# Optimization experiments

Measured on AMD Instinct MI355X. Metric: run time of the kernel, lower is better.

Reference implementation:

```python
import jax, jax.numpy as jnp
import numpy as np

# norse LIFParameters defaults with v_th overridden to 0.33
DT = 1e-3
TAU_SYN_INV = 200.0   # 1/5e-3
TAU_MEM_INV = 100.0   # 1/1e-2
V_TH = 0.33
ALPHA = 100.0         # SuperSpike surrogate slope
SEQ_LEN = 32

@jax.custom_vjp
def superspike(x):
    # Heaviside forward, SuperSpike surrogate backward (norse method='super')
    return (x > 0).astype(x.dtype)

def _ss_fwd(x):
    return superspike(x), x

def _ss_bwd(x, g):
    return (g / (ALPHA * jnp.abs(x) + 1.0) ** 2,)

superspike.defvjp(_ss_fwd, _ss_bwd)

def _encode(current):
    # ConstantCurrentLIFEncoder: LIF current encoder, constant input current
    def step(v, _):
        v = v + DT * TAU_MEM_INV * (-v + current)
        z = superspike(v - V_TH)
        v = v - z * v  # v_reset = 0
        return v, z
    _, spikes = jax.lax.scan(step, jnp.zeros_like(current), None, length=SEQ_LEN)
    return spikes  # [T, B, F]

def _lif_step(inp, v, i):
    # norse lif_feed_forward_step (v_leak=0, v_reset=0)
    v_dec = v + DT * TAU_MEM_INV * (-v + i)
    i_dec = i * (1.0 - DT * TAU_SYN_INV)
    z = superspike(v_dec - V_TH)
    return z, v_dec * (1.0 - z), i_dec + inp

def setup_inputs() -> dict:
    key = jax.random.key(0)
    ks = jax.random.split(key, 6)
    B, F_IN, N_CLASSES = 2048, 2048, 100  # F_IN = 2*input_size
    def lin_w(k, out_f, in_f):
        bound = 1.0 / np.sqrt(in_f)
        return jax.random.uniform(k, (out_f, in_f), jnp.float32, -bound, bound)
    return {
        "x": jax.random.normal(ks[0], (B, F_IN), jnp.float32),
        "w1": lin_w(ks[1], 512, F_IN),
        "w2": lin_w(ks[2], 512, 512),
        "w3": lin_w(ks[3], 256, 512),
        "w_out": lin_w(ks[4], N_CLASSES, 256),
        "feature_scalar": jnp.ones((1,), jnp.float32),
        "encoder_scalar": jnp.ones((1,), jnp.float32),
    }

def reference(x, w1, w2, w3, w_out, feature_scalar, encoder_scalar):
    B = x.shape[0]
    n_classes = w_out.shape[0]
    # encoder + scaling (dropout is identity in eval mode)
    spikes = 5.0 * encoder_scalar * _encode(2.0 * feature_scalar * x)  # [T,B,F]

    def step(carry, z_t):
        v1, i1, v2, i2, v3, i3, vo, io = carry
        s1, v1, i1 = _lif_step(z_t @ w1.T, v1, i1)
        s2, v2, i2 = _lif_step(s1 @ w2.T, v2, i2)
        s3, v3, i3 = _lif_step(s2 @ w3.T, v3, i3)
        # LILinearCell (leaky integrator, no spike)
        vo = vo + DT * TAU_MEM_INV * (-vo + io)
        io = io * (1.0 - DT * TAU_SYN_INV) + s3 @ w_out.T
        return (v1, i1, v2, i2, v3, i3, vo, io), None

    z = lambda *s: jnp.zeros(s, x.dtype)
    init = (z(B, 512), z(B, 512), z(B, 512), z(B, 512),
            z(B, 256), z(B, 256), z(B, n_classes), z(B, n_classes))
    final, _ = jax.lax.scan(step, init, spikes)
    # decode = voltages[-1] == LI membrane voltage at last timestep
    return final[6]
```

## Files before the change

kernel.cpp:

```cpp
#include <hip/hip_runtime.h>
#include <cstddef>


#define THREADS 256

typedef float f4v __attribute__((ext_vector_type(4)));
typedef float f2v __attribute__((ext_vector_type(2)));

__device__ __forceinline__ void gl_lds16(const float* g, float* l) {
#if __has_builtin(__builtin_amdgcn_global_load_lds)
  __builtin_amdgcn_global_load_lds(
      (const __attribute__((address_space(1))) void*)g,
      (__attribute__((address_space(3))) void*)l, 16, 0, 0);
#else
  *(float4*)l = *(const float4*)g;
#endif
}

#define WOFF1 0
#define WOFF2 1048576
#define WOFF3 1310720
#define WOFF4 1441792
#define WTOT  1474560

__global__ __launch_bounds__(THREADS) void prep_kernel(
    const float* __restrict__ w1, const float* __restrict__ w2,
    const float* __restrict__ w3, const float* __restrict__ w4,
    float* __restrict__ wt)
{
  int idx = blockIdx.x * THREADS + threadIdx.x;
  if (idx >= WTOT) return;
  if (idx < WOFF2) {
    int j = idx >> 9, o = idx & 511;
    wt[idx] = w1[o * 2048 + j];
  } else if (idx < WOFF3) {
    int r = idx - WOFF2, j = r >> 9, o = r & 511;
    wt[idx] = w2[o * 512 + j];
  } else if (idx < WOFF4) {
    int r = idx - WOFF3, j = r >> 8, o = r & 255;
    wt[idx] = w3[o * 512 + j];
  } else {
    int r = idx - WOFF4, j = r >> 7, o = r & 127;
    wt[idx] = (o < 100) ? w4[o * 256 + j] : 0.0f;
  }
}

__global__ __launch_bounds__(THREADS) void enc_kernel(
    const float* __restrict__ x, const float* __restrict__ fscale,
    unsigned* __restrict__ em, int b0)
{
  int idx = blockIdx.x * THREADS + threadIdx.x;
  int b = idx >> 11, j = idx & 2047;
  float c = 2.0f * fscale[0] * x[((size_t)(b0 + b) << 11) + j];
  float v = 0.0f;
  unsigned m = 0u;
#pragma unroll
  for (int t = 0; t < 32; ++t) {
    v = v + 0.1f * (c - v);
    unsigned z = ((v - 0.33f) > 0.0f) ? 1u : 0u;
    m |= z << t;
    if (z) v = 0.0f;
  }
  em[idx] = m;
}

template <int O, bool FINAL>
__global__ __launch_bounds__(THREADS, 2) void gemm_sparse(
    const unsigned* __restrict__ mIn, const float* __restrict__ WT,
    int J, const float* __restrict__ es,
    unsigned* __restrict__ mOut, float* __restrict__ out, int bbase)
{
  constexpr int NAO = (O >= 256) ? 4 : 2;
  constexpr int WPB = O / (64 * NAO);
  constexpr int BPB = 4 / WPB;
  constexpr int BK  = 8192 / O;
  constexpr int CH  = 8192;
  static_assert(BK % 4 == 0, "uint4 mask loads");
  __shared__ float lds[2 * CH];
  const int tid = threadIdx.x;
  const int lane = tid & 63, wvid = tid >> 6;
  const int b = blockIdx.x * BPB + wvid / WPB;
  const int obase = (wvid % WPB) * (64 * NAO) + lane * NAO;
  const int nb = J / BK;
  float scalef = es ? 5.0f * es[0] : 1.0f;
  const int scale_i =
      __builtin_amdgcn_readfirstlane(__float_as_int(scalef));
  float* const buf0 = lds;
  float* const buf1 = lds + CH;

  float acc[32][NAO];
#pragma unroll
  for (int t = 0; t < 32; ++t)
#pragma unroll
    for (int k = 0; k < NAO; ++k) acc[t][k] = 0.0f;

  const unsigned* mrow = mIn + (size_t)b * J;

  auto stage = [&](int cb, float* buf) {
#pragma unroll
    for (int i = 0; i < CH / THREADS / 4; ++i) {
      int flat = (tid + i * THREADS) * 4;
      gl_lds16(WT + (size_t)cb * CH + flat, buf + flat);
    }
  };

  auto fma_chunk = [&](int cb, const float* buf) {
    uint4 mw[BK / 4];
#pragma unroll
    for (int q = 0; q < BK / 4; ++q)
      mw[q] = ((const uint4*)(mrow + cb * BK))[q];
    unsigned mwa[BK];
#pragma unroll
    for (int q = 0; q < BK / 4; ++q) {
      mwa[4 * q + 0] = mw[q].x; mwa[4 * q + 1] = mw[q].y;
      mwa[4 * q + 2] = mw[q].z; mwa[4 * q + 3] = mw[q].w;
    }
#pragma unroll
    for (int j = 0; j < BK; ++j) {
      const unsigned w =
          (unsigned)__builtin_amdgcn_readfirstlane((int)mwa[j]);
      if (w) {
        if constexpr (NAO == 4) {
          const f4v wv = *(const f4v*)(buf + j * O + obase);
#pragma unroll
          for (int t = 0; t < 32; ++t) {
            float av = __int_as_float(
                (int)((((int)(w << (31 - t))) >> 31) & scale_i));
#pragma unroll
            for (int k = 0; k < 4; ++k)
              acc[t][k] = fmaf(av, wv[k], acc[t][k]);
          }
        } else {
          const f2v wv = *(const f2v*)(buf + j * O + obase);
#pragma unroll
          for (int t = 0; t < 32; ++t) {
            float av = __int_as_float(
                (int)((((int)(w << (31 - t))) >> 31) & scale_i));
#pragma unroll
            for (int k = 0; k < 2; ++k)
              acc[t][k] = fmaf(av, wv[k], acc[t][k]);
          }
        }
      }
    }
  };

  stage(0, buf0);
  for (int cb = 0; cb < nb; cb += 2) {
    __syncthreads();
    if (cb + 1 < nb) stage(cb + 1, buf1);
    fma_chunk(cb, buf0);
    __syncthreads();
    if (cb + 2 < nb) stage(cb + 2, buf0);
    fma_chunk(cb + 1, buf1);
  }

#pragma unroll
  for (int k = 0; k < NAO; ++k) {
    if (FINAL) {
      float v = 0.0f, cur = 0.0f;
#pragma unroll
      for (int t2 = 0; t2 < 32; ++t2) {
        v = v + 0.1f * (cur - v);
        cur = 0.8f * cur + acc[t2][k];
      }
      int o = obase + k;
      if (o < 100) out[(size_t)(bbase + b) * 100 + o] = v;
    } else {
      float v = 0.0f, cur = 0.0f;
      unsigned zw = 0u;
#pragma unroll
      for (int t2 = 0; t2 < 32; ++t2) {
        v = v + 0.1f * (cur - v);
        unsigned z = ((v - 0.33f) > 0.0f) ? 1u : 0u;
        zw |= z << t2;
        if (z) v = 0.0f;
        cur = 0.8f * cur + acc[t2][k];
      }
      mOut[(size_t)b * O + obase + k] = zw;
    }
  }
}

extern "C" void kernel_launch(void* const* d_in, const int* in_sizes, int n_in,
                              void* d_out, int out_size, void* d_ws, size_t ws_size,
                              hipStream_t stream)
{
  const float* x  = (const float*)d_in[0];
  const float* w1 = (const float*)d_in[1];
  const float* w2 = (const float*)d_in[2];
  const float* w3 = (const float*)d_in[3];
  const float* w4 = (const float*)d_in[4];
  const float* fs = (const float*)d_in[5];
  const float* es = (const float*)d_in[6];
  float* out = (float*)d_out;
  (void)in_sizes; (void)n_in; (void)out_size;

  int Bc = 2048;
  auto need = [](int bc) -> size_t {
    return ((size_t)WTOT + (size_t)bc * (2048 + 512 + 512 + 256)) * 4;
  };
  while (Bc > 64 && need(Bc) > ws_size) Bc >>= 1;

  float* WT = (float*)d_ws;
  unsigned* em  = (unsigned*)(WT + WTOT);
  unsigned* s1m = em  + (size_t)Bc * 2048;
  unsigned* s2m = s1m + (size_t)Bc * 512;
  unsigned* s3m = s2m + (size_t)Bc * 512;

  prep_kernel<<<(WTOT + THREADS - 1) / THREADS, THREADS, 0, stream>>>(
      w1, w2, w3, w4, WT);

  for (int b0 = 0; b0 < 2048; b0 += Bc) {
    enc_kernel<<<(Bc * 2048) / THREADS, THREADS, 0, stream>>>(x, fs, em, b0);
    gemm_sparse<512, false><<<Bc / 2, THREADS, 0, stream>>>(
        em, WT + WOFF1, 2048, es, s1m, nullptr, 0);
    gemm_sparse<512, false><<<Bc / 2, THREADS, 0, stream>>>(
        s1m, WT + WOFF2, 512, nullptr, s2m, nullptr, 0);
    gemm_sparse<256, false><<<Bc / 4, THREADS, 0, stream>>>(
        s2m, WT + WOFF3, 512, nullptr, s3m, nullptr, 0);
    gemm_sparse<128, true><<<Bc / 4, THREADS, 0, stream>>>(
        s3m, WT + WOFF4, 256, nullptr, nullptr, out, b0);
  }
}
```

Before: 1.191 ms.

## Load weight rows directly from global memory only for active inputs

New measurement: 1.204 ms. Within noise of the previous version (+1.2%).

```diff
diff --git a/kernel.cpp b/kernel.cpp
--- a/kernel.cpp
+++ b/kernel.cpp
@@ -6,16 +6,6 @@
 
 typedef float f4v __attribute__((ext_vector_type(4)));
 typedef float f2v __attribute__((ext_vector_type(2)));
-
-__device__ __forceinline__ void gl_lds16(const float* g, float* l) {
-#if __has_builtin(__builtin_amdgcn_global_load_lds)
-  __builtin_amdgcn_global_load_lds(
-      (const __attribute__((address_space(1))) void*)g,
-      (__attribute__((address_space(3))) void*)l, 16, 0, 0);
-#else
-  *(float4*)l = *(const float4*)g;
-#endif
-}
 
 #define WOFF1 0
 #define WOFF2 1048576
@@ -73,20 +63,15 @@
   constexpr int NAO = (O >= 256) ? 4 : 2;
   constexpr int WPB = O / (64 * NAO);
   constexpr int BPB = 4 / WPB;
-  constexpr int BK  = 8192 / O;
-  constexpr int CH  = 8192;
-  static_assert(BK % 4 == 0, "uint4 mask loads");
-  __shared__ float lds[2 * CH];
+  typedef float fv __attribute__((ext_vector_type(NAO)));
   const int tid = threadIdx.x;
   const int lane = tid & 63, wvid = tid >> 6;
   const int b = blockIdx.x * BPB + wvid / WPB;
   const int obase = (wvid % WPB) * (64 * NAO) + lane * NAO;
-  const int nb = J / BK;
+  const float* const wbase = WT + obase;
   float scalef = es ? 5.0f * es[0] : 1.0f;
   const int scale_i =
       __builtin_amdgcn_readfirstlane(__float_as_int(scalef));
-  float* const buf0 = lds;
-  float* const buf1 = lds + CH;
 
   float acc[32][NAO];
 #pragma unroll
@@ -96,63 +81,32 @@
 
   const unsigned* mrow = mIn + (size_t)b * J;
 
-  auto stage = [&](int cb, float* buf) {
+  for (int j0 = 0; j0 < J; j0 += 4) {
+    const uint4 mq = *(const uint4*)(mrow + j0);
+    unsigned w[4];
+    w[0] = (unsigned)__builtin_amdgcn_readfirstlane((int)mq.x);
+    w[1] = (unsigned)__builtin_amdgcn_readfirstlane((int)mq.y);
+    w[2] = (unsigned)__builtin_amdgcn_readfirstlane((int)mq.z);
+    w[3] = (unsigned)__builtin_amdgcn_readfirstlane((int)mq.w);
+
+    fv wv[4];
 #pragma unroll
-    for (int i = 0; i < CH / THREADS / 4; ++i) {
-      int flat = (tid + i * THREADS) * 4;
-      gl_lds16(WT + (size_t)cb * CH + flat, buf + flat);
-    }
-  };
+    for (int jj = 0; jj < 4; ++jj)
+      if (w[jj]) wv[jj] = *(const fv*)(wbase + (size_t)(j0 + jj) * O);
 
-  auto fma_chunk = [&](int cb, const float* buf) {
-    uint4 mw[BK / 4];
 #pragma unroll
-    for (int q = 0; q < BK / 4; ++q)
-      mw[q] = ((const uint4*)(mrow + cb * BK))[q];
-    unsigned mwa[BK];
+    for (int jj = 0; jj < 4; ++jj) {
+      if (w[jj]) {
 #pragma unroll
-    for (int q = 0; q < BK / 4; ++q) {
-      mwa[4 * q + 0] = mw[q].x; mwa[4 * q + 1] = mw[q].y;
-      mwa[4 * q + 2] = mw[q].z; mwa[4 * q + 3] = mw[q].w;
-    }
+        for (int t = 0; t < 32; ++t) {
+          float av = __int_as_float(
+              (int)((((int)(w[jj] << (31 - t))) >> 31) & scale_i));
 #pragma unroll
-    for (int j = 0; j < BK; ++j) {
-      const unsigned w =
-          (unsigned)__builtin_amdgcn_readfirstlane((int)mwa[j]);
-      if (w) {
-        if constexpr (NAO == 4) {
-          const f4v wv = *(const f4v*)(buf + j * O + obase);
-#pragma unroll
-          for (int t = 0; t < 32; ++t) {
-            float av = __int_as_float(
-                (int)((((int)(w << (31 - t))) >> 31) & scale_i));
-#pragma unroll
-            for (int k = 0; k < 4; ++k)
-              acc[t][k] = fmaf(av, wv[k], acc[t][k]);
-          }
-        } else {
-          const f2v wv = *(const f2v*)(buf + j * O + obase);
-#pragma unroll
-          for (int t = 0; t < 32; ++t) {
-            float av = __int_as_float(
-                (int)((((int)(w << (31 - t))) >> 31) & scale_i));
-#pragma unroll
-            for (int k = 0; k < 2; ++k)
-              acc[t][k] = fmaf(av, wv[k], acc[t][k]);
-          }
+          for (int k = 0; k < NAO; ++k)
+            acc[t][k] = fmaf(av, wv[jj][k], acc[t][k]);
         }
       }
     }
-  };
-
-  stage(0, buf0);
-  for (int cb = 0; cb < nb; cb += 2) {
-    __syncthreads();
-    if (cb + 1 < nb) stage(cb + 1, buf1);
-    fma_chunk(cb, buf0);
-    __syncthreads();
-    if (cb + 2 < nb) stage(cb + 2, buf0);
-    fma_chunk(cb + 1, buf1);
   }
 
 #pragma unroll
```
